# Optimization experiments

Measured on AMD Instinct MI355X. Metric: run time of the kernel, lower is better.

## Reference

```python
import jax, jax.numpy as jnp
import numpy as np

N_NODES = 100000
N_EDGES = 1600000
F_IN = 128
HID = 128


def setup_inputs() -> dict:
    key = jax.random.key(0)
    ks = jax.random.split(key, 16)
    x = jax.random.normal(ks[0], (N_NODES, F_IN), dtype=jnp.float32)
    edge_index = jax.random.randint(ks[1], (2, N_EDGES), 0, N_NODES, dtype=jnp.int32)
    edge_weight = jax.random.uniform(ks[2], (N_EDGES,), dtype=jnp.float32)
    def glorot(k, fan_in, fan_out):
        s = jnp.sqrt(6.0 / (fan_in + fan_out))
        return jax.random.uniform(k, (fan_in, fan_out), dtype=jnp.float32, minval=-s, maxval=s)
    inp = {"x": x, "edge_index": edge_index, "edge_weight": edge_weight}
    dims = [(F_IN, HID), (HID, HID), (HID, HID), (HID, HID)]
    for i, (di, do) in enumerate(dims):
        inp[f"Wc{i}"] = glorot(ks[3 + i], di, do)
        inp[f"bc{i}"] = jnp.zeros((do,), dtype=jnp.float32)
    inp["Wout"] = glorot(ks[8], HID, F_IN)
    inp["bout"] = jnp.zeros((F_IN,), dtype=jnp.float32)
    return inp


def _gcn_conv(x, W, b, row, col, ew, deg_isqrt, n):
    # PyG GCNConv: h = x @ W; out = sum_{(r,c)} norm_rc * h[r] scattered to c, plus
    # self-loop term (weight 1), plus bias. norm_rc = d^-1/2[r] * ew * d^-1/2[c].
    h = x @ W
    norm = deg_isqrt[row] * ew * deg_isqrt[col]          # [E]
    agg = jax.ops.segment_sum(h[row] * norm[:, None], col, num_segments=n)
    agg = agg + h * (deg_isqrt * deg_isqrt)[:, None]      # self loops, weight 1
    return agg + b


def reference(x, edge_index, edge_weight, Wc0, bc0, Wc1, bc1, Wc2, bc2, Wc3, bc3, Wout, bout):
    n = x.shape[0]
    row, col = edge_index[0], edge_index[1]
    # degree includes self-loop weight 1 (gcn_norm with add_self_loops=True)
    deg = jax.ops.segment_sum(edge_weight, col, num_segments=n) + 1.0
    deg_isqrt = jnp.where(deg > 0, jax.lax.rsqrt(deg), 0.0)
    Ws = [Wc0, Wc1, Wc2, Wc3]
    bs = [bc0, bc1, bc2, bc3]
    h = x
    for i in range(3):
        h = jax.nn.relu(_gcn_conv(h, Ws[i], bs[i], row, col, edge_weight, deg_isqrt, n))
    h = _gcn_conv(h, Ws[3], bs[3], row, col, edge_weight, deg_isqrt, n)
    return h @ Wout + bout
```

## Files before the change

### kernel.cpp

```cpp
#include <hip/hip_runtime.h>


#define SCAN_CHUNK 1024
#define NBUCK_MAX  512
#define BCAP       6144

typedef __attribute__((ext_vector_type(8))) short bf16x8;
typedef __attribute__((ext_vector_type(4))) float f32x4;

__device__ inline unsigned bf16pack(float a, float b) {
    unsigned ua = __float_as_uint(a);
    unsigned ub = __float_as_uint(b);
    ua = (ua + 0x7fffu + ((ua >> 16) & 1u)) >> 16;
    ub = (ub + 0x7fffu + ((ub >> 16) & 1u)) & 0xffff0000u;
    return ua | ub;
}

__device__ inline void split2(float x, ushort& hi, ushort& lo) {
    unsigned u = __float_as_uint(x);
    unsigned r = (u + 0x7fffu + ((u >> 16) & 1u)) & 0xffff0000u;
    hi = (ushort)(r >> 16);
    float rem = x - __uint_as_float(r);
    unsigned u2 = __float_as_uint(rem);
    lo = (ushort)((u2 + 0x7fffu + ((u2 >> 16) & 1u)) >> 16);
}

__device__ inline void bf16x8_expand(uint4 w, float4& a, float4& b) {
    a.x = __uint_as_float(w.x << 16);
    a.y = __uint_as_float(w.x & 0xffff0000u);
    a.z = __uint_as_float(w.y << 16);
    a.w = __uint_as_float(w.y & 0xffff0000u);
    b.x = __uint_as_float(w.z << 16);
    b.y = __uint_as_float(w.z & 0xffff0000u);
    b.z = __uint_as_float(w.w << 16);
    b.w = __uint_as_float(w.w & 0xffff0000u);
}

__global__ __launch_bounds__(256) void k_prepw(const float* W0, const float* W1,
                                               const float* W2, const float* W3,
                                               const float* W4,
                                               ushort* __restrict__ hiO,
                                               ushort* __restrict__ loO) {
    const float* W = (blockIdx.x == 0) ? W0 : (blockIdx.x == 1) ? W1 :
                     (blockIdx.x == 2) ? W2 : (blockIdx.x == 3) ? W3 : W4;
    ushort* h = hiO + (size_t)blockIdx.x * 16384;
    ushort* l = loO + (size_t)blockIdx.x * 16384;
    for (int idx = threadIdx.x; idx < 4096; idx += 256) {
        int n  = idx >> 5;
        int kq = (idx & 31) * 4;
        ushort hs[4], ls[4];
#pragma unroll
        for (int j = 0; j < 4; j++) split2(W[(kq + j) * 128 + n], hs[j], ls[j]);
        *(uint2*)&h[n * 128 + kq] =
            make_uint2(hs[0] | ((unsigned)hs[1] << 16), hs[2] | ((unsigned)hs[3] << 16));
        *(uint2*)&l[n * 128 + kq] =
            make_uint2(ls[0] | ((unsigned)ls[1] << 16), ls[2] | ((unsigned)ls[3] << 16));
    }
}

__global__ __launch_bounds__(256) void k_hist(const int* __restrict__ col,
                                              int* __restrict__ hist,
                                              int E, int K, int B1, int chunk) {
    __shared__ int cnt[NBUCK_MAX];
    int b = blockIdx.x, t = threadIdx.x;
    for (int k = t; k < K; k += 256) cnt[k] = 0;
    __syncthreads();
    int e0 = b * chunk, e1 = min(e0 + chunk, E);
    for (int e = e0 + t; e < e1; e += 256) atomicAdd(&cnt[col[e] >> 8], 1);
    __syncthreads();
    for (int k = t; k < K; k += 256) hist[k * B1 + b] = cnt[k];
}

__global__ __launch_bounds__(256) void k_scan_part(const int* __restrict__ count,
                                                   int* __restrict__ partials, int n) {
    __shared__ int red[256];
    int t = threadIdx.x;
    int base = blockIdx.x * SCAN_CHUNK + t * 4;
    int s = 0;
#pragma unroll
    for (int j = 0; j < 4; j++) {
        int i = base + j;
        if (i < n) s += count[i];
    }
    red[t] = s;
    __syncthreads();
    for (int off = 128; off > 0; off >>= 1) {
        if (t < off) red[t] += red[t + off];
        __syncthreads();
    }
    if (t == 0) partials[blockIdx.x] = red[0];
}

__global__ __launch_bounds__(1024) void k_scan_top(const int* __restrict__ partials,
                                                   int* __restrict__ blockOff,
                                                   int* __restrict__ result,
                                                   int nb, int n) {
    __shared__ int sums[1024];
    int t = threadIdx.x;
    int v = (t < nb) ? partials[t] : 0;
    sums[t] = v;
    __syncthreads();
    for (int off = 1; off < 1024; off <<= 1) {
        int u = (t >= off) ? sums[t - off] : 0;
        __syncthreads();
        sums[t] += u;
        __syncthreads();
    }
    if (t < nb) blockOff[t] = sums[t] - v;
    if (t == nb - 1) result[n] = sums[t];
}

__global__ __launch_bounds__(256) void k_scan_out(const int* __restrict__ count,
                                                  const int* __restrict__ blockOff,
                                                  int* __restrict__ result, int n) {
    __shared__ int sums[256];
    int t = threadIdx.x;
    int base = blockIdx.x * SCAN_CHUNK + t * 4;
    int c[4]; int s = 0;
#pragma unroll
    for (int j = 0; j < 4; j++) {
        int i = base + j;
        c[j] = (i < n) ? count[i] : 0;
        s += c[j];
    }
    sums[t] = s;
    __syncthreads();
    for (int off = 1; off < 256; off <<= 1) {
        int u = (t >= off) ? sums[t - off] : 0;
        __syncthreads();
        sums[t] += u;
        __syncthreads();
    }
    int run = blockOff[blockIdx.x] + sums[t] - s;
#pragma unroll
    for (int j = 0; j < 4; j++) {
        int i = base + j;
        if (i < n) result[i] = run;
        run += c[j];
    }
}

__global__ __launch_bounds__(256) void k_scatter(const int* __restrict__ row,
                                                 const int* __restrict__ col,
                                                 const float* __restrict__ ew,
                                                 const int* __restrict__ binBase,
                                                 uint2* __restrict__ etmp,
                                                 int E, int K, int B1, int chunk) {
    __shared__ int cur[NBUCK_MAX];
    int b = blockIdx.x, t = threadIdx.x;
    for (int k = t; k < K; k += 256) cur[k] = binBase[k * B1 + b];
    __syncthreads();
    int e0 = b * chunk, e1 = min(e0 + chunk, E);
    for (int e = e0 + t; e < e1; e += 256) {
        int c = col[e];
        int k = c >> 8;
        int pos = atomicAdd(&cur[k], 1);
        etmp[pos] = make_uint2((unsigned)row[e] | ((unsigned)(c & 255) << 24),
                               __float_as_uint(ew[e]));
    }
}

__global__ __launch_bounds__(256) void k_bucket(const uint2* __restrict__ etmp,
                                                const int* __restrict__ binBase,
                                                uint2* __restrict__ edges,
                                                int* __restrict__ offsets,
                                                float* __restrict__ disq,
                                                int N, int K, int B1) {
    __shared__ unsigned ls[BCAP];
    __shared__ unsigned lw[BCAP];
    __shared__ int   cnt[256];
    __shared__ float sew[256];
    __shared__ int   excl[257];
    int k = blockIdx.x, t = threadIdx.x;
    int bStart = binBase[k * B1];
    int bEnd   = binBase[(k + 1) * B1];
    int size   = bEnd - bStart;
    cnt[t] = 0; sew[t] = 0.f;
    __syncthreads();
    for (int i = t; i < size && i < BCAP; i += 256) {
        uint2 m = etmp[bStart + i];
        ls[i] = m.x; lw[i] = m.y;
        int j = m.x >> 24;
        atomicAdd(&cnt[j], 1);
        atomicAdd(&sew[j], __uint_as_float(m.y));
    }
    __syncthreads();
    excl[t + 1] = cnt[t];
    if (t == 0) excl[0] = 0;
    __syncthreads();
    for (int off = 1; off < 256; off <<= 1) {
        int add = (t + 1 > off) ? excl[t + 1 - off] : 0;
        __syncthreads();
        excl[t + 1] += add;
        __syncthreads();
    }
    int node = (k << 8) + t;
    if (node < N) {
        offsets[node] = bStart + excl[t];
        disq[node]    = rsqrtf(1.0f + sew[t]);
    }
    if (k == K - 1 && t == 0) offsets[N] = bEnd;
    cnt[t] = excl[t];
    __syncthreads();
    for (int i = t; i < size && i < BCAP; i += 256) {
        unsigned s = ls[i];
        int j = s >> 24;
        int pos = atomicAdd(&cnt[j], 1);
        edges[bStart + pos] = make_uint2((s & 0x00FFFFFFu) << 8, lw[i]);
    }
}

__global__ __launch_bounds__(256) void k_gemm_f32A(const float* __restrict__ A,
                                                   const ushort* __restrict__ WThi,
                                                   const ushort* __restrict__ WTlo,
                                                   const float* __restrict__ disq,
                                                   unsigned* __restrict__ Cout, int N) {
    __shared__ ushort Whi_s[128][136];
    __shared__ ushort Wlo_s[128][136];
    int tid = threadIdx.x;
#pragma unroll
    for (int r = 0; r < 8; r++) {
        int n  = r * 16 + (tid >> 4);
        int kq = (tid & 15) * 8;
        *(uint4*)&Whi_s[n][kq] = *(const uint4*)&WThi[n * 128 + kq];
        *(uint4*)&Wlo_s[n][kq] = *(const uint4*)&WTlo[n * 128 + kq];
    }
    __syncthreads();

    int wv = tid >> 6, ln = tid & 63;
    int quad = ln >> 4, col = ln & 15;
    int nodeBase = blockIdx.x * 128 + wv * 32;
    int node0 = nodeBase + col, node1 = nodeBase + 16 + col;

    f32x4 acc[2][8];
#pragma unroll
    for (int nb = 0; nb < 2; nb++)
#pragma unroll
        for (int f = 0; f < 8; f++) acc[nb][f] = (f32x4)0.f;

    for (int s = 0; s < 4; s++) {
        int k0 = s * 32 + quad * 8;
        float v0[8], v1[8];
#pragma unroll
        for (int j = 0; j < 8; j++) { v0[j] = 0.f; v1[j] = 0.f; }
        if (node0 < N) {
            float4 a = *(const float4*)&A[(size_t)node0 * 128 + k0];
            float4 b = *(const float4*)&A[(size_t)node0 * 128 + k0 + 4];
            v0[0] = a.x; v0[1] = a.y; v0[2] = a.z; v0[3] = a.w;
            v0[4] = b.x; v0[5] = b.y; v0[6] = b.z; v0[7] = b.w;
        }
        if (node1 < N) {
            float4 a = *(const float4*)&A[(size_t)node1 * 128 + k0];
            float4 b = *(const float4*)&A[(size_t)node1 * 128 + k0 + 4];
            v1[0] = a.x; v1[1] = a.y; v1[2] = a.z; v1[3] = a.w;
            v1[4] = b.x; v1[5] = b.y; v1[6] = b.z; v1[7] = b.w;
        }
        bf16x8 bh0, bl0, bh1, bl1;
#pragma unroll
        for (int j = 0; j < 8; j++) {
            ushort h, l;
            split2(v0[j], h, l); bh0[j] = (short)h; bl0[j] = (short)l;
            split2(v1[j], h, l); bh1[j] = (short)h; bl1[j] = (short)l;
        }
#pragma unroll
        for (int f = 0; f < 8; f++) {
            bf16x8 wh = *(const bf16x8*)&Whi_s[f * 16 + col][k0];
            bf16x8 wl = *(const bf16x8*)&Wlo_s[f * 16 + col][k0];
            acc[0][f] = __builtin_amdgcn_mfma_f32_16x16x32_bf16(wh, bh0, acc[0][f], 0, 0, 0);
            acc[1][f] = __builtin_amdgcn_mfma_f32_16x16x32_bf16(wh, bh1, acc[1][f], 0, 0, 0);
            acc[0][f] = __builtin_amdgcn_mfma_f32_16x16x32_bf16(wl, bh0, acc[0][f], 0, 0, 0);
            acc[1][f] = __builtin_amdgcn_mfma_f32_16x16x32_bf16(wl, bh1, acc[1][f], 0, 0, 0);
            acc[0][f] = __builtin_amdgcn_mfma_f32_16x16x32_bf16(wh, bl0, acc[0][f], 0, 0, 0);
            acc[1][f] = __builtin_amdgcn_mfma_f32_16x16x32_bf16(wh, bl1, acc[1][f], 0, 0, 0);
        }
    }
#pragma unroll
    for (int nb = 0; nb < 2; nb++) {
        int node = nodeBase + nb * 16 + col;
        if (node >= N) continue;
        float d = disq[node];
#pragma unroll
        for (int f = 0; f < 8; f++) {
            f32x4 a = acc[nb][f];
            uint2 u;
            u.x = bf16pack(a[0] * d, a[1] * d);
            u.y = bf16pack(a[2] * d, a[3] * d);
            *(uint2*)&Cout[(size_t)node * 64 + f * 8 + quad * 2] = u;
        }
    }
}

template <bool BF16OUT>
__global__ __launch_bounds__(256) void k_gemm_b16A(const unsigned* __restrict__ Ab,
                                                   const ushort* __restrict__ WThi,
                                                   const ushort* __restrict__ WTlo,
                                                   const float* __restrict__ bias,
                                                   const float* __restrict__ disq,
                                                   void* __restrict__ Cout, int N) {
    __shared__ ushort Whi_s[128][136];
    __shared__ ushort Wlo_s[128][136];
    int tid = threadIdx.x;
#pragma unroll
    for (int r = 0; r < 8; r++) {
        int n  = r * 16 + (tid >> 4);
        int kq = (tid & 15) * 8;
        *(uint4*)&Whi_s[n][kq] = *(const uint4*)&WThi[n * 128 + kq];
        *(uint4*)&Wlo_s[n][kq] = *(const uint4*)&WTlo[n * 128 + kq];
    }
    __syncthreads();

    int wv = tid >> 6, ln = tid & 63;
    int quad = ln >> 4, col = ln & 15;
    int nodeBase = blockIdx.x * 128 + wv * 32;
    int node0 = nodeBase + col, node1 = nodeBase + 16 + col;

    f32x4 acc[2][8];
#pragma unroll
    for (int nb = 0; nb < 2; nb++)
#pragma unroll
        for (int f = 0; f < 8; f++) acc[nb][f] = (f32x4)0.f;

    for (int s = 0; s < 4; s++) {
        int k0 = s * 32 + quad * 8;
        int kw = s * 16 + quad * 4;
        bf16x8 b0 = (bf16x8)(short)0, b1 = (bf16x8)(short)0;
        if (node0 < N) b0 = *(const bf16x8*)&Ab[(size_t)node0 * 64 + kw];
        if (node1 < N) b1 = *(const bf16x8*)&Ab[(size_t)node1 * 64 + kw];
#pragma unroll
        for (int f = 0; f < 8; f++) {
            bf16x8 wh = *(const bf16x8*)&Whi_s[f * 16 + col][k0];
            bf16x8 wl = *(const bf16x8*)&Wlo_s[f * 16 + col][k0];
            acc[0][f] = __builtin_amdgcn_mfma_f32_16x16x32_bf16(wh, b0, acc[0][f], 0, 0, 0);
            acc[1][f] = __builtin_amdgcn_mfma_f32_16x16x32_bf16(wh, b1, acc[1][f], 0, 0, 0);
            acc[0][f] = __builtin_amdgcn_mfma_f32_16x16x32_bf16(wl, b0, acc[0][f], 0, 0, 0);
            acc[1][f] = __builtin_amdgcn_mfma_f32_16x16x32_bf16(wl, b1, acc[1][f], 0, 0, 0);
        }
    }
#pragma unroll
    for (int nb = 0; nb < 2; nb++) {
        int node = nodeBase + nb * 16 + col;
        if (node >= N) continue;
        if (BF16OUT) {
            float d = disq[node];
            unsigned* tb = (unsigned*)Cout;
#pragma unroll
            for (int f = 0; f < 8; f++) {
                f32x4 a = acc[nb][f];
                uint2 u;
                u.x = bf16pack(a[0] * d, a[1] * d);
                u.y = bf16pack(a[2] * d, a[3] * d);
                *(uint2*)&tb[(size_t)node * 64 + f * 8 + quad * 2] = u;
            }
        } else {
            float* C = (float*)Cout;
#pragma unroll
            for (int f = 0; f < 8; f++) {
                int fb = f * 16 + quad * 4;
                float4 bv = *(const float4*)&bias[fb];
                f32x4 a = acc[nb][f];
                float4 o;
                o.x = a[0] + bv.x; o.y = a[1] + bv.y;
                o.z = a[2] + bv.z; o.w = a[3] + bv.w;
                *(float4*)&C[(size_t)node * 128 + fb] = o;
            }
        }
    }
}

__global__ __launch_bounds__(256, 4) void k_aggregate(const unsigned* __restrict__ tb,
                                                      const int* __restrict__ offsets,
                                                      const uint2* __restrict__ edges,
                                                      const float* __restrict__ disq,
                                                      const float* __restrict__ bias,
                                                      unsigned* __restrict__ outb,
                                                      int N, int relu) {
    const int tid = threadIdx.x;
    const int wv = tid >> 6, lane = tid & 63;
    const int q = lane >> 4, li = lane & 15;
    const int node = blockIdx.x * 16 + wv * 4 + q;
    if (node >= N) return;
    const char* tbc = (const char*)tb;

    int e0 = offsets[node], e1 = offsets[node + 1];
    float4 acc0 = make_float4(0.f, 0.f, 0.f, 0.f);
    float4 acc1 = make_float4(0.f, 0.f, 0.f, 0.f);

    uint2 md[8]; float cf[8]; uint4 w[8];

#define META(S, II) {                                                      \
        int ii = (II);                                                     \
        md[S] = (ii < e1) ? edges[ii] : make_uint2(0u, 0u);                \
    }
#define GATHER(S) {                                                        \
        cf[S] = __uint_as_float(md[S].y);                                  \
        w[S]  = *(const uint4*)(tbc + md[S].x + (li << 4));                \
    }
#define CONSUME(S) {                                                       \
        float4 a, b; bf16x8_expand(w[S], a, b);                            \
        float c = cf[S];                                                   \
        acc0.x += c * a.x; acc0.y += c * a.y;                              \
        acc0.z += c * a.z; acc0.w += c * a.w;                              \
        acc1.x += c * b.x; acc1.y += c * b.y;                              \
        acc1.z += c * b.z; acc1.w += c * b.w;                              \
    }

    META(0, e0)     META(1, e0 + 1) META(2, e0 + 2) META(3, e0 + 3)
    META(4, e0 + 4) META(5, e0 + 5) META(6, e0 + 6) META(7, e0 + 7)
    GATHER(0) GATHER(1) GATHER(2) GATHER(3)
    GATHER(4) GATHER(5) GATHER(6) GATHER(7)
    META(0, e0 + 8)  META(1, e0 + 9)  META(2, e0 + 10) META(3, e0 + 11)
    META(4, e0 + 12) META(5, e0 + 13) META(6, e0 + 14) META(7, e0 + 15)

    for (int eb = e0 + 8; eb < e1; eb += 8) {
        CONSUME(0) GATHER(0) META(0, eb + 8)
        CONSUME(1) GATHER(1) META(1, eb + 9)
        CONSUME(2) GATHER(2) META(2, eb + 10)
        CONSUME(3) GATHER(3) META(3, eb + 11)
        CONSUME(4) GATHER(4) META(4, eb + 12)
        CONSUME(5) GATHER(5) META(5, eb + 13)
        CONSUME(6) GATHER(6) META(6, eb + 14)
        CONSUME(7) GATHER(7) META(7, eb + 15)
    }
    CONSUME(0) CONSUME(1) CONSUME(2) CONSUME(3)
    CONSUME(4) CONSUME(5) CONSUME(6) CONSUME(7)
#undef META
#undef GATHER
#undef CONSUME

    float d = disq[node];
    uint4 sv = *(const uint4*)(tbc + ((size_t)node << 8) + (li << 4));
    float4 ta, tbv;
    bf16x8_expand(sv, ta, tbv);
    float4 b0 = *(const float4*)&bias[li * 8];
    float4 b1 = *(const float4*)&bias[li * 8 + 4];
    float4 o0, o1;
    o0.x = d * (acc0.x + ta.x) + b0.x;
    o0.y = d * (acc0.y + ta.y) + b0.y;
    o0.z = d * (acc0.z + ta.z) + b0.z;
    o0.w = d * (acc0.w + ta.w) + b0.w;
    o1.x = d * (acc1.x + tbv.x) + b1.x;
    o1.y = d * (acc1.y + tbv.y) + b1.y;
    o1.z = d * (acc1.z + tbv.z) + b1.z;
    o1.w = d * (acc1.w + tbv.w) + b1.w;
    if (relu) {
        o0.x = fmaxf(o0.x, 0.f); o0.y = fmaxf(o0.y, 0.f);
        o0.z = fmaxf(o0.z, 0.f); o0.w = fmaxf(o0.w, 0.f);
        o1.x = fmaxf(o1.x, 0.f); o1.y = fmaxf(o1.y, 0.f);
        o1.z = fmaxf(o1.z, 0.f); o1.w = fmaxf(o1.w, 0.f);
    }
    uint4 u;
    u.x = bf16pack(o0.x, o0.y);
    u.y = bf16pack(o0.z, o0.w);
    u.z = bf16pack(o1.x, o1.y);
    u.w = bf16pack(o1.z, o1.w);
    *(uint4*)&outb[(size_t)node * 64 + li * 4] = u;
}

extern "C" void kernel_launch(void* const* d_in, const int* in_sizes, int n_in,
                              void* d_out, int out_size, void* d_ws, size_t ws_size,
                              hipStream_t stream) {
    const float* x    = (const float*)d_in[0];
    const int*   ei   = (const int*)d_in[1];
    const float* ew   = (const float*)d_in[2];
    const float* Wc[4] = {(const float*)d_in[3], (const float*)d_in[5],
                          (const float*)d_in[7], (const float*)d_in[9]};
    const float* bc[4] = {(const float*)d_in[4], (const float*)d_in[6],
                          (const float*)d_in[8], (const float*)d_in[10]};
    const float* Wout = (const float*)d_in[11];
    const float* bout = (const float*)d_in[12];

    const int N = in_sizes[0] / 128;
    const int E = in_sizes[2];
    const int* row = ei;
    const int* col = ei + E;

    const int K     = (N + 255) >> 8;
    const int B1    = 256;
    const int chunk = (E + B1 - 1) / B1;
    const int nScan = K * B1;

    size_t off = 0;
    char* base = (char*)d_ws;
    auto alloc = [&](size_t bytes) -> void* {
        void* p = base + off;
        off += (bytes + 255) & ~(size_t)255;
        return p;
    };
    float*    disq     = (float*)alloc((size_t)N * 4);
    int*      offsets  = (int*)alloc((size_t)(N + 1) * 4);
    int*      hist     = (int*)alloc((size_t)nScan * 4);
    int*      binBase  = (int*)alloc((size_t)(nScan + 1) * 4);
    int*      partials = (int*)alloc(1024 * 4);
    int*      blockOff = (int*)alloc(1024 * 4);
    ushort*   WThi     = (ushort*)alloc((size_t)5 * 16384 * 2);
    ushort*   WTlo     = (ushort*)alloc((size_t)5 * 16384 * 2);
    uint2*    etmp     = (uint2*)alloc((size_t)E * 8);
    uint2*    edges    = (uint2*)alloc((size_t)E * 8);
    unsigned* hb       = (unsigned*)alloc((size_t)N * 64 * 4);
    unsigned* tb       = (unsigned*)alloc((size_t)N * 64 * 4);

    const int BG  = (N + 127) / 128;
    const int BA  = (N + 15) / 16;
    const int NBs = (nScan + SCAN_CHUNK - 1) / SCAN_CHUNK;

    k_prepw<<<5, 256, 0, stream>>>(Wc[0], Wc[1], Wc[2], Wc[3], Wout, WThi, WTlo);
    k_hist<<<B1, 256, 0, stream>>>(col, hist, E, K, B1, chunk);
    k_scan_part<<<NBs, 256, 0, stream>>>(hist, partials, nScan);
    k_scan_top<<<1, 1024, 0, stream>>>(partials, blockOff, binBase, NBs, nScan);
    k_scan_out<<<NBs, 256, 0, stream>>>(hist, blockOff, binBase, nScan);
    k_scatter<<<B1, 256, 0, stream>>>(row, col, ew, binBase, etmp, E, K, B1, chunk);
    k_bucket<<<K, 256, 0, stream>>>(etmp, binBase, edges, offsets, disq, N, K, B1);

    k_gemm_f32A<<<BG, 256, 0, stream>>>(x, WThi, WTlo, disq, tb, N);
    k_aggregate<<<BA, 256, 0, stream>>>(tb, offsets, edges, disq, bc[0], hb, N, 1);
    k_gemm_b16A<true><<<BG, 256, 0, stream>>>(hb, WThi + 16384, WTlo + 16384, nullptr, disq, tb, N);
    k_aggregate<<<BA, 256, 0, stream>>>(tb, offsets, edges, disq, bc[1], hb, N, 1);
    k_gemm_b16A<true><<<BG, 256, 0, stream>>>(hb, WThi + 32768, WTlo + 32768, nullptr, disq, tb, N);
    k_aggregate<<<BA, 256, 0, stream>>>(tb, offsets, edges, disq, bc[2], hb, N, 1);
    k_gemm_b16A<true><<<BG, 256, 0, stream>>>(hb, WThi + 49152, WTlo + 49152, nullptr, disq, tb, N);
    k_aggregate<<<BA, 256, 0, stream>>>(tb, offsets, edges, disq, bc[3], hb, N, 0);
    k_gemm_b16A<false><<<BG, 256, 0, stream>>>(hb, WThi + 65536, WTlo + 65536, bout, nullptr, d_out, N);
}
```

Measured before the change: 582.5 us.

## Fuse neighbor aggregation with the following layer GEMM in one kernel

Merges each aggregate kernel with the next layer's GEMM. A block aggregates 16 nodes into shared memory as bf16, then runs MFMA against the next weight matrix. The bf16 weights are read directly from global memory (L2) instead of being staged in LDS. This removes four kernel launches and the round trip of the intermediate hidden buffer through HBM. The cost is that every 16-node block re-reads the full weight split, and the per-wave GEMM tile is small.

```diff
diff --git a/kernel.cpp b/kernel.cpp
--- a/kernel.cpp
+++ b/kernel.cpp
@@ -290,98 +290,26 @@
     }
 }
 
-template <bool BF16OUT>
-__global__ __launch_bounds__(256) void k_gemm_b16A(const unsigned* __restrict__ Ab,
+template <int FINAL>
+__global__ __launch_bounds__(256, 4) void k_fusedL(const unsigned* __restrict__ tbIn,
                                                    const ushort* __restrict__ WThi,
                                                    const ushort* __restrict__ WTlo,
-                                                   const float* __restrict__ bias,
+                                                   const float* __restrict__ aggBias,
+                                                   const float* __restrict__ outBias,
                                                    const float* __restrict__ disq,
-                                                   void* __restrict__ Cout, int N) {
-    __shared__ ushort Whi_s[128][136];
-    __shared__ ushort Wlo_s[128][136];
-    int tid = threadIdx.x;
-#pragma unroll
-    for (int r = 0; r < 8; r++) {
-        int n  = r * 16 + (tid >> 4);
-        int kq = (tid & 15) * 8;
-        *(uint4*)&Whi_s[n][kq] = *(const uint4*)&WThi[n * 128 + kq];
-        *(uint4*)&Wlo_s[n][kq] = *(const uint4*)&WTlo[n * 128 + kq];
-    }
-    __syncthreads();
-
-    int wv = tid >> 6, ln = tid & 63;
-    int quad = ln >> 4, col = ln & 15;
-    int nodeBase = blockIdx.x * 128 + wv * 32;
-    int node0 = nodeBase + col, node1 = nodeBase + 16 + col;
-
-    f32x4 acc[2][8];
-#pragma unroll
-    for (int nb = 0; nb < 2; nb++)
-#pragma unroll
-        for (int f = 0; f < 8; f++) acc[nb][f] = (f32x4)0.f;
-
-    for (int s = 0; s < 4; s++) {
-        int k0 = s * 32 + quad * 8;
-        int kw = s * 16 + quad * 4;
-        bf16x8 b0 = (bf16x8)(short)0, b1 = (bf16x8)(short)0;
-        if (node0 < N) b0 = *(const bf16x8*)&Ab[(size_t)node0 * 64 + kw];
-        if (node1 < N) b1 = *(const bf16x8*)&Ab[(size_t)node1 * 64 + kw];
-#pragma unroll
-        for (int f = 0; f < 8; f++) {
-            bf16x8 wh = *(const bf16x8*)&Whi_s[f * 16 + col][k0];
-            bf16x8 wl = *(const bf16x8*)&Wlo_s[f * 16 + col][k0];
-            acc[0][f] = __builtin_amdgcn_mfma_f32_16x16x32_bf16(wh, b0, acc[0][f], 0, 0, 0);
-            acc[1][f] = __builtin_amdgcn_mfma_f32_16x16x32_bf16(wh, b1, acc[1][f], 0, 0, 0);
-            acc[0][f] = __builtin_amdgcn_mfma_f32_16x16x32_bf16(wl, b0, acc[0][f], 0, 0, 0);
-            acc[1][f] = __builtin_amdgcn_mfma_f32_16x16x32_bf16(wl, b1, acc[1][f], 0, 0, 0);
-        }
-    }
-#pragma unroll
-    for (int nb = 0; nb < 2; nb++) {
-        int node = nodeBase + nb * 16 + col;
-        if (node >= N) continue;
-        if (BF16OUT) {
-            float d = disq[node];
-            unsigned* tb = (unsigned*)Cout;
-#pragma unroll
-            for (int f = 0; f < 8; f++) {
-                f32x4 a = acc[nb][f];
-                uint2 u;
-                u.x = bf16pack(a[0] * d, a[1] * d);
-                u.y = bf16pack(a[2] * d, a[3] * d);
-                *(uint2*)&tb[(size_t)node * 64 + f * 8 + quad * 2] = u;
-            }
-        } else {
-            float* C = (float*)Cout;
-#pragma unroll
-            for (int f = 0; f < 8; f++) {
-                int fb = f * 16 + quad * 4;
-                float4 bv = *(const float4*)&bias[fb];
-                f32x4 a = acc[nb][f];
-                float4 o;
-                o.x = a[0] + bv.x; o.y = a[1] + bv.y;
-                o.z = a[2] + bv.z; o.w = a[3] + bv.w;
-                *(float4*)&C[(size_t)node * 128 + fb] = o;
-            }
-        }
-    }
-}
-
-__global__ __launch_bounds__(256, 4) void k_aggregate(const unsigned* __restrict__ tb,
-                                                      const int* __restrict__ offsets,
-                                                      const uint2* __restrict__ edges,
-                                                      const float* __restrict__ disq,
-                                                      const float* __restrict__ bias,
-                                                      unsigned* __restrict__ outb,
-                                                      int N, int relu) {
+                                                   const int* __restrict__ offsets,
+                                                   const uint2* __restrict__ edges,
+                                                   void* __restrict__ outp, int N) {
+    __shared__ __align__(16) ushort hsm[16 * 128];
     const int tid = threadIdx.x;
     const int wv = tid >> 6, lane = tid & 63;
     const int q = lane >> 4, li = lane & 15;
-    const int node = blockIdx.x * 16 + wv * 4 + q;
-    if (node >= N) return;
-    const char* tbc = (const char*)tb;
-
-    int e0 = offsets[node], e1 = offsets[node + 1];
+    const int nl = wv * 4 + q;
+    const int node = blockIdx.x * 16 + nl;
+    const char* tbc = (const char*)tbIn;
+
+    int e0 = 0, e1 = 0;
+    if (node < N) { e0 = offsets[node]; e1 = offsets[node + 1]; }
     float4 acc0 = make_float4(0.f, 0.f, 0.f, 0.f);
     float4 acc1 = make_float4(0.f, 0.f, 0.f, 0.f);
 
@@ -427,33 +355,82 @@
 #undef GATHER
 #undef CONSUME
 
-    float d = disq[node];
-    uint4 sv = *(const uint4*)(tbc + ((size_t)node << 8) + (li << 4));
-    float4 ta, tbv;
-    bf16x8_expand(sv, ta, tbv);
-    float4 b0 = *(const float4*)&bias[li * 8];
-    float4 b1 = *(const float4*)&bias[li * 8 + 4];
-    float4 o0, o1;
-    o0.x = d * (acc0.x + ta.x) + b0.x;
-    o0.y = d * (acc0.y + ta.y) + b0.y;
-    o0.z = d * (acc0.z + ta.z) + b0.z;
-    o0.w = d * (acc0.w + ta.w) + b0.w;
-    o1.x = d * (acc1.x + tbv.x) + b1.x;
-    o1.y = d * (acc1.y + tbv.y) + b1.y;
-    o1.z = d * (acc1.z + tbv.z) + b1.z;
-    o1.w = d * (acc1.w + tbv.w) + b1.w;
-    if (relu) {
-        o0.x = fmaxf(o0.x, 0.f); o0.y = fmaxf(o0.y, 0.f);
-        o0.z = fmaxf(o0.z, 0.f); o0.w = fmaxf(o0.w, 0.f);
-        o1.x = fmaxf(o1.x, 0.f); o1.y = fmaxf(o1.y, 0.f);
-        o1.z = fmaxf(o1.z, 0.f); o1.w = fmaxf(o1.w, 0.f);
-    }
-    uint4 u;
-    u.x = bf16pack(o0.x, o0.y);
-    u.y = bf16pack(o0.z, o0.w);
-    u.z = bf16pack(o1.x, o1.y);
-    u.w = bf16pack(o1.z, o1.w);
-    *(uint4*)&outb[(size_t)node * 64 + li * 4] = u;
+    if (node < N) {
+        float d = disq[node];
+        uint4 sv = *(const uint4*)(tbc + ((size_t)node << 8) + (li << 4));
+        float4 ta, tbv;
+        bf16x8_expand(sv, ta, tbv);
+        float4 b0 = *(const float4*)&aggBias[li * 8];
+        float4 b1 = *(const float4*)&aggBias[li * 8 + 4];
+        float4 o0, o1;
+        o0.x = d * (acc0.x + ta.x) + b0.x;
+        o0.y = d * (acc0.y + ta.y) + b0.y;
+        o0.z = d * (acc0.z + ta.z) + b0.z;
+        o0.w = d * (acc0.w + ta.w) + b0.w;
+        o1.x = d * (acc1.x + tbv.x) + b1.x;
+        o1.y = d * (acc1.y + tbv.y) + b1.y;
+        o1.z = d * (acc1.z + tbv.z) + b1.z;
+        o1.w = d * (acc1.w + tbv.w) + b1.w;
+        if (!FINAL) {
+            o0.x = fmaxf(o0.x, 0.f); o0.y = fmaxf(o0.y, 0.f);
+            o0.z = fmaxf(o0.z, 0.f); o0.w = fmaxf(o0.w, 0.f);
+            o1.x = fmaxf(o1.x, 0.f); o1.y = fmaxf(o1.y, 0.f);
+            o1.z = fmaxf(o1.z, 0.f); o1.w = fmaxf(o1.w, 0.f);
+        }
+        uint4 u;
+        u.x = bf16pack(o0.x, o0.y);
+        u.y = bf16pack(o0.z, o0.w);
+        u.z = bf16pack(o1.x, o1.y);
+        u.w = bf16pack(o1.z, o1.w);
+        *(uint4*)&hsm[nl * 128 + ((li ^ (nl & 7)) << 3)] = u;
+    }
+    __syncthreads();
+
+    f32x4 ag0 = (f32x4)0.f, ag1 = (f32x4)0.f;
+    for (int s = 0; s < 4; s++) {
+        int k0 = s * 32 + q * 8;
+        const ushort* wr = WThi + (wv * 32 + li) * 128 + k0;
+        const ushort* wr2 = WTlo + (wv * 32 + li) * 128 + k0;
+        bf16x8 wh0 = *(const bf16x8*)wr;
+        bf16x8 wh1 = *(const bf16x8*)(wr + 2048);
+        bf16x8 wl0 = *(const bf16x8*)wr2;
+        bf16x8 wl1 = *(const bf16x8*)(wr2 + 2048);
+        int slot = (s * 4 + q) ^ (li & 7);
+        bf16x8 b = *(const bf16x8*)&hsm[li * 128 + slot * 8];
+        ag0 = __builtin_amdgcn_mfma_f32_16x16x32_bf16(wh0, b, ag0, 0, 0, 0);
+        ag0 = __builtin_amdgcn_mfma_f32_16x16x32_bf16(wl0, b, ag0, 0, 0, 0);
+        ag1 = __builtin_amdgcn_mfma_f32_16x16x32_bf16(wh1, b, ag1, 0, 0, 0);
+        ag1 = __builtin_amdgcn_mfma_f32_16x16x32_bf16(wl1, b, ag1, 0, 0, 0);
+    }
+
+    int nodeOut = blockIdx.x * 16 + li;
+    if (nodeOut < N) {
+        if (!FINAL) {
+            float d = disq[nodeOut];
+            unsigned* tbo = (unsigned*)outp;
+            uint2 u0, u1;
+            u0.x = bf16pack(ag0[0] * d, ag0[1] * d);
+            u0.y = bf16pack(ag0[2] * d, ag0[3] * d);
+            u1.x = bf16pack(ag1[0] * d, ag1[1] * d);
+            u1.y = bf16pack(ag1[2] * d, ag1[3] * d);
+            int f0 = wv * 2;
+            *(uint2*)&tbo[(size_t)nodeOut * 64 + f0 * 8 + q * 2] = u0;
+            *(uint2*)&tbo[(size_t)nodeOut * 64 + (f0 + 1) * 8 + q * 2] = u1;
+        } else {
+            float* C = (float*)outp;
+            int fb0 = (wv * 2) * 16 + q * 4;
+            int fb1 = (wv * 2 + 1) * 16 + q * 4;
+            float4 bv0 = *(const float4*)&outBias[fb0];
+            float4 bv1 = *(const float4*)&outBias[fb1];
+            float4 o0, o1;
+            o0.x = ag0[0] + bv0.x; o0.y = ag0[1] + bv0.y;
+            o0.z = ag0[2] + bv0.z; o0.w = ag0[3] + bv0.w;
+            o1.x = ag1[0] + bv1.x; o1.y = ag1[1] + bv1.y;
+            o1.z = ag1[2] + bv1.z; o1.w = ag1[3] + bv1.w;
+            *(float4*)&C[(size_t)nodeOut * 128 + fb0] = o0;
+            *(float4*)&C[(size_t)nodeOut * 128 + fb1] = o1;
+        }
+    }
 }
 
 extern "C" void kernel_launch(void* const* d_in, const int* in_sizes, int n_in,
@@ -496,11 +473,11 @@
     ushort*   WTlo     = (ushort*)alloc((size_t)5 * 16384 * 2);
     uint2*    etmp     = (uint2*)alloc((size_t)E * 8);
     uint2*    edges    = (uint2*)alloc((size_t)E * 8);
-    unsigned* hb       = (unsigned*)alloc((size_t)N * 64 * 4);
-    unsigned* tb       = (unsigned*)alloc((size_t)N * 64 * 4);
+    unsigned* bufA     = (unsigned*)alloc((size_t)N * 64 * 4);
+    unsigned* bufB     = (unsigned*)alloc((size_t)N * 64 * 4);
 
     const int BG  = (N + 127) / 128;
-    const int BA  = (N + 15) / 16;
+    const int BF  = (N + 15) / 16;
     const int NBs = (nScan + SCAN_CHUNK - 1) / SCAN_CHUNK;
 
     k_prepw<<<5, 256, 0, stream>>>(Wc[0], Wc[1], Wc[2], Wc[3], Wout, WThi, WTlo);
@@ -511,13 +488,13 @@
     k_scatter<<<B1, 256, 0, stream>>>(row, col, ew, binBase, etmp, E, K, B1, chunk);
     k_bucket<<<K, 256, 0, stream>>>(etmp, binBase, edges, offsets, disq, N, K, B1);
 
-    k_gemm_f32A<<<BG, 256, 0, stream>>>(x, WThi, WTlo, disq, tb, N);
-    k_aggregate<<<BA, 256, 0, stream>>>(tb, offsets, edges, disq, bc[0], hb, N, 1);
-    k_gemm_b16A<true><<<BG, 256, 0, stream>>>(hb, WThi + 16384, WTlo + 16384, nullptr, disq, tb, N);
-    k_aggregate<<<BA, 256, 0, stream>>>(tb, offsets, edges, disq, bc[1], hb, N, 1);
-    k_gemm_b16A<true><<<BG, 256, 0, stream>>>(hb, WThi + 32768, WTlo + 32768, nullptr, disq, tb, N);
-    k_aggregate<<<BA, 256, 0, stream>>>(tb, offsets, edges, disq, bc[2], hb, N, 1);
-    k_gemm_b16A<true><<<BG, 256, 0, stream>>>(hb, WThi + 49152, WTlo + 49152, nullptr, disq, tb, N);
-    k_aggregate<<<BA, 256, 0, stream>>>(tb, offsets, edges, disq, bc[3], hb, N, 0);
-    k_gemm_b16A<false><<<BG, 256, 0, stream>>>(hb, WThi + 65536, WTlo + 65536, bout, nullptr, d_out, N);
-}
+    k_gemm_f32A<<<BG, 256, 0, stream>>>(x, WThi, WTlo, disq, bufA, N);
+    k_fusedL<0><<<BF, 256, 0, stream>>>(bufA, WThi + 16384, WTlo + 16384,
+                                        bc[0], nullptr, disq, offsets, edges, bufB, N);
+    k_fusedL<0><<<BF, 256, 0, stream>>>(bufB, WThi + 32768, WTlo + 32768,
+                                        bc[1], nullptr, disq, offsets, edges, bufA, N);
+    k_fusedL<0><<<BF, 256, 0, stream>>>(bufA, WThi + 49152, WTlo + 49152,
+                                        bc[2], nullptr, disq, offsets, edges, bufB, N);
+    k_fusedL<1><<<BF, 256, 0, stream>>>(bufB, WThi + 65536, WTlo + 65536,
+                                        bc[3], bout, disq, offsets, edges, d_out, N);
+}
```

Result: slower. 677.3 us (+16.3%).
